# Kernel tuning notes

Hardware: AMD Instinct MI355X
Metric: run time of the kernel (lower is better)

## Reference

```python
import jax, jax.numpy as jnp
import numpy as np
from jax import lax

V_PATCH = (1, 4, 16, 64, 256, 1024)  # must end at L
RESI = 0.5    # quant_resi ratio inside Phi
BETA = 0.25
K_PHI = 4     # share_quant_resi


def _phi_indices():
    # PhiPartiallyShared tick lookup, resolved statically per scale
    K = K_PHI
    ticks = np.linspace(1/3/K, 1 - 1/3/K, K) if K == 4 else np.linspace(1/2/K, 1 - 1/2/K, K)
    SN = len(V_PATCH)
    return [int(np.argmin(np.abs(ticks - (si / (SN - 1) if SN > 1 else 0.0)))) for si in range(SN)]


def interp_linear(x, Lo):
    # torch F.interpolate(mode='linear', align_corners=False) on last axis of [B,C,Li]
    Li = x.shape[-1]
    if Li == Lo:
        return x
    pos = (jnp.arange(Lo, dtype=jnp.float32) + 0.5) * (Li / Lo) - 0.5
    pos = jnp.clip(pos, 0.0, Li - 1)
    lo = jnp.floor(pos).astype(jnp.int32)
    hi = jnp.minimum(lo + 1, Li - 1)
    w = pos - lo.astype(jnp.float32)
    return x[..., lo] * (1.0 - w) + x[..., hi] * w


def phi_apply(h, w, b):
    # Phi: h*(1-r) + Conv1d(ks=3,pad=1)(h)*r
    y = lax.conv_general_dilated(h, w, (1,), [(1, 1)], dimension_numbers=('NCH', 'OIH', 'NCH'))
    y = y + b[None, :, None]
    return h * (1.0 - RESI) + y * RESI


def reference(f_BCL, emb, phi_w, phi_b):
    f = f_BCL.astype(jnp.float32)
    B, C, L = f.shape
    f_ng = lax.stop_gradient(f)
    f_rest = f_ng
    f_hat = jnp.zeros_like(f_ng)
    SN = len(V_PATCH)
    pidx = _phi_indices()
    e_sq = jnp.sum(emb * emb, axis=1)  # [V]
    loss = jnp.float32(0.0)
    for si, pl in enumerate(V_PATCH):
        rest = interp_linear(f_rest, pl) if si != SN - 1 else f_rest
        z = rest.transpose(0, 2, 1).reshape(-1, C)              # [B*pl, C]
        d = jnp.sum(z * z, axis=1, keepdims=True) + e_sq - 2.0 * (z @ emb.T)  # [B*pl, V]
        idx = jnp.argmin(d, axis=1)
        h = emb[idx].reshape(B, pl, C).transpose(0, 2, 1)        # [B,C,pl]
        if si != SN - 1:
            h = interp_linear(h, L)
        h = phi_apply(h, phi_w[pidx[si]], phi_b[pidx[si]])
        f_hat = f_hat + h
        f_rest = f_rest - h
        loss = loss + BETA * jnp.mean((lax.stop_gradient(f_hat) - f) ** 2) \
                    + jnp.mean((f_hat - f_ng) ** 2)
    loss = loss / SN
    # straight-through estimator
    f_hat_st = lax.stop_gradient(f_hat) - f_ng + f
    return f_hat_st, loss


def setup_inputs() -> dict:
    key = jax.random.key(0)
    k1, k2, k3 = jax.random.split(key, 3)
    B, C, L, V = 32, 32, 1024, 4096
    f_BCL = jax.random.normal(k1, (B, C, L), dtype=jnp.float32)
    emb = jax.random.normal(k2, (V, C), dtype=jnp.float32)
    phi_w = jax.random.normal(k3, (K_PHI, C, C, 3), dtype=jnp.float32) * 0.05
    phi_b = jnp.zeros((K_PHI, C), dtype=jnp.float32)
    return {"f_BCL": f_BCL, "emb": emb, "phi_w": phi_w, "phi_b": phi_b}
```

## Files before the change

kernel.cpp:

```cpp
#include <hip/hip_runtime.h>
#include <stdint.h>

#define BDIM 32
#define CDIM 32
#define LDIM 1024
#define VDIM 4096
#define BCL (BDIM*CDIM*LDIM)

typedef _Float16 f16x8 __attribute__((ext_vector_type(8)));
typedef float f32x4 __attribute__((ext_vector_type(4)));

#define PIN_V(x) asm volatile("" : "+v"(x))

__global__ void init_kernel(const float* __restrict__ f, const float* __restrict__ emb,
                            float* __restrict__ f_rest, float* __restrict__ f_hat,
                            float* __restrict__ e_sq,
                            _Float16* __restrict__ eh, _Float16* __restrict__ el,
                            float* __restrict__ loss_acc, unsigned* __restrict__ done_ctr,
                            unsigned long long* __restrict__ keys, int nkeys) {
    int i = blockIdx.x * blockDim.x + threadIdx.x;
    if (i < BCL) { f_rest[i] = f[i]; f_hat[i] = 0.0f; }
    if (i < VDIM) {
        const float* e = emb + (size_t)i * CDIM;
        float s = 0.f;
#pragma unroll
        for (int k = 0; k < 32; ++k) {
            float v = e[k];
            s = fmaf(v, v, s);
            if (eh) {
                _Float16 h = (_Float16)v;
                float r = v - (float)h;
                eh[(size_t)i*32 + k] = (_Float16)(-2.0f) * h;
                el[(size_t)i*32 + k] = (_Float16)(-2.0f) * (_Float16)r;
            }
        }
        e_sq[i] = s;
    }
    if (i < nkeys) keys[i] = ~0ull;
    if (i == 0) { *loss_acc = 0.f; *done_ctr = 0u; }
}

__global__ __launch_bounds__(256) void vq_mfma(
    const _Float16* __restrict__ z_hi, const _Float16* __restrict__ z_lo,
    const _Float16* __restrict__ e_hi, const _Float16* __restrict__ e_lo,
    const float* __restrict__ e_sq, unsigned long long* __restrict__ keys,
    int NQ, int VC, int vchunks, int vsub)
{
    const int t = threadIdx.x;
    const int lane = t & 63;
    const int w = t >> 6;
    const int qg = blockIdx.x / vchunks;
    const int vc = blockIdx.x % vchunks;
    const int vb0 = vc * (vsub * VC);

    __shared__ __align__(16) _Float16 eh_ls[256*32];
    __shared__ __align__(16) _Float16 el_ls[256*32];
    __shared__ float esq_ls[256];

    const int fr = lane & 15;
    const int kq = lane >> 4;
    const int qbase = qg*256 + w*64;
    f16x8 ah[4], al[4];
#pragma unroll
    for (int tq = 0; tq < 4; ++tq) {
        int q = qbase + tq*16 + fr;
        ah[tq] = *(const f16x8*)(z_hi + (size_t)q*32 + kq*8);
        al[tq] = *(const f16x8*)(z_lo + (size_t)q*32 + kq*8);
    }

    float bd[4][4]; int bv[4][4];
#pragma unroll
    for (int tq = 0; tq < 4; ++tq)
#pragma unroll
        for (int i = 0; i < 4; ++i) { bd[tq][i] = 3.4e38f; bv[tq][i] = 0; }

    for (int sub = 0; sub < vsub; ++sub) {
        const int vb = vb0 + sub * VC;

        {
            const float4* sH = (const float4*)(e_hi + (size_t)vb*32);
            const float4* sL = (const float4*)(e_lo + (size_t)vb*32);
            float4* dH = (float4*)eh_ls; float4* dL = (float4*)el_ls;
            int n4 = VC * 4;
            for (int x = t; x < n4; x += 256) {
                int row = x >> 2, c = x & 3;
                int ds = row*4 + (c ^ ((row >> 1) & 3));
                dH[ds] = sH[x]; dL[ds] = sL[x];
            }
            for (int v = t; v < VC; v += 256) esq_ls[v] = e_sq[vb + v];
        }
        __syncthreads();

        for (int vt = 0; vt < VC; vt += 16) {
            const int row = vt + fr;
            const int koff = (kq ^ ((row >> 1) & 3)) * 8;
            const f16x8 bh = *(const f16x8*)(eh_ls + (size_t)row*32 + koff);
            const f16x8 bl = *(const f16x8*)(el_ls + (size_t)row*32 + koff);
            float es = esq_ls[row];
            int vg = vb + row;
#pragma unroll
            for (int tq = 0; tq < 4; ++tq) {
                f32x4 acc = {es, es, es, es};
                acc = __builtin_amdgcn_mfma_f32_16x16x32_f16(ah[tq], bh, acc, 0,0,0);
                acc = __builtin_amdgcn_mfma_f32_16x16x32_f16(ah[tq], bl, acc, 0,0,0);
                acc = __builtin_amdgcn_mfma_f32_16x16x32_f16(al[tq], bh, acc, 0,0,0);
#pragma unroll
                for (int i = 0; i < 4; ++i)
                    if (acc[i] < bd[tq][i]) { bd[tq][i] = acc[i]; bv[tq][i] = vg; }
            }
        }
        __syncthreads();
    }

#pragma unroll
    for (int tq = 0; tq < 4; ++tq) {
#pragma unroll
        for (int i = 0; i < 4; ++i) {
            unsigned u = __float_as_uint(bd[tq][i]);
            u = (u & 0x80000000u) ? ~u : (u | 0x80000000u);
            unsigned long long k = ((unsigned long long)u << 32) | (unsigned)bv[tq][i];
#pragma unroll
            for (int m = 1; m < 16; m <<= 1) {
                unsigned long long o = __shfl_xor(k, m, 64); if (o < k) k = o;
            }
            if (fr == 0) {
                int q = qbase + tq*16 + kq*4 + i;
                atomicMin(&keys[q], k);
            }
        }
    }
}

__global__ __launch_bounds__(256) void vq_scan(
    const float* __restrict__ f_rest, const float* __restrict__ z_buf,
    const float* __restrict__ emb, const float* __restrict__ e_sq,
    unsigned long long* __restrict__ keys,
    int lpl, int s, int NQ, int VC, int vchunks)
{
    const int pl = 1 << lpl;
    const int t  = threadIdx.x;
    const int qg = blockIdx.x / vchunks;
    const int vc = blockIdx.x % vchunks;
    const int vb = vc * VC;

    __shared__ __align__(16) float e_ls[128 * 32];
    __shared__ float esq_ls[128];

    {
        const float4* src = (const float4*)emb + (size_t)vb * 8;
        float4* dst = (float4*)e_ls;
        for (int x = t; x < VC * 8; x += 256) dst[x] = src[x];
        if (t < VC) esq_ls[t] = e_sq[vb + t];
    }

    const int q0 = qg * 512 + t;
    const int q1 = q0 + 256;
    const int qc0 = (q0 < NQ) ? q0 : NQ - 1;
    const int qc1 = (q1 < NQ) ? q1 : NQ - 1;

    float z0[32], z1[32];
    if (z_buf) {
        const float4* p0 = (const float4*)(z_buf + (size_t)qc0 * 32);
        const float4* p1 = (const float4*)(z_buf + (size_t)qc1 * 32);
#pragma unroll
        for (int c4 = 0; c4 < 8; ++c4) {
            float4 a = p0[c4], b = p1[c4];
            z0[c4*4+0] = a.x; z0[c4*4+1] = a.y; z0[c4*4+2] = a.z; z0[c4*4+3] = a.w;
            z1[c4*4+0] = b.x; z1[c4*4+1] = b.y; z1[c4*4+2] = b.z; z1[c4*4+3] = b.w;
        }
    } else {
        int b0 = qc0 >> lpl, j0 = qc0 & (pl - 1);
        int b1 = qc1 >> lpl, j1 = qc1 & (pl - 1);
        if (pl == LDIM) {
            const float* p0 = f_rest + b0 * (CDIM * LDIM) + j0;
            const float* p1 = f_rest + b1 * (CDIM * LDIM) + j1;
#pragma unroll
            for (int c = 0; c < 32; ++c) { z0[c] = p0[c * LDIM]; z1[c] = p1[c * LDIM]; }
        } else {
            int col0 = j0 * s + (s >> 1) - 1;
            int col1 = j1 * s + (s >> 1) - 1;
            const float* p0 = f_rest + b0 * (CDIM * LDIM) + col0;
            const float* p1 = f_rest + b1 * (CDIM * LDIM) + col1;
#pragma unroll
            for (int c = 0; c < 32; ++c) {
                z0[c] = 0.5f * (p0[c * LDIM] + p0[c * LDIM + 1]);
                z1[c] = 0.5f * (p1[c * LDIM] + p1[c * LDIM + 1]);
            }
        }
    }

    __syncthreads();

    float bd0 = 3.4e38f, bd1 = 3.4e38f;
    int bv0 = 0, bv1 = 0;

#pragma unroll 1
    for (int v = 0; v < VC; v += 2) {
#pragma unroll
        for (int c = 0; c < 32; ++c) { PIN_V(z0[c]); PIN_V(z1[c]); }

        const float4* er0 = (const float4*)&e_ls[(size_t)v * 32];
        const float4* er1 = er0 + 8;
        float es0 = esq_ls[v];
        float es1 = esq_ls[v + 1];

        float4 e0 = er0[0], e1 = er1[0];
        float a00 = z0[0] * e0.x,        a01 = z0[0] * e1.x;
        float a10 = z1[0] * e0.x,        a11 = z1[0] * e1.x;
        a00 = fmaf(z0[1], e0.y, a00);    a01 = fmaf(z0[1], e1.y, a01);
        a10 = fmaf(z1[1], e0.y, a10);    a11 = fmaf(z1[1], e1.y, a11);
        a00 = fmaf(z0[2], e0.z, a00);    a01 = fmaf(z0[2], e1.z, a01);
        a10 = fmaf(z1[2], e0.z, a10);    a11 = fmaf(z1[2], e1.z, a11);
        a00 = fmaf(z0[3], e0.w, a00);    a01 = fmaf(z0[3], e1.w, a01);
        a10 = fmaf(z1[3], e0.w, a10);    a11 = fmaf(z1[3], e1.w, a11);
#pragma unroll
        for (int c4 = 1; c4 < 8; ++c4) {
            e0 = er0[c4]; e1 = er1[c4];
            a00 = fmaf(z0[c4*4+0], e0.x, a00);  a01 = fmaf(z0[c4*4+0], e1.x, a01);
            a10 = fmaf(z1[c4*4+0], e0.x, a10);  a11 = fmaf(z1[c4*4+0], e1.x, a11);
            a00 = fmaf(z0[c4*4+1], e0.y, a00);  a01 = fmaf(z0[c4*4+1], e1.y, a01);
            a10 = fmaf(z1[c4*4+1], e0.y, a10);  a11 = fmaf(z1[c4*4+1], e1.y, a11);
            a00 = fmaf(z0[c4*4+2], e0.z, a00);  a01 = fmaf(z0[c4*4+2], e1.z, a01);
            a10 = fmaf(z1[c4*4+2], e0.z, a10);  a11 = fmaf(z1[c4*4+2], e1.z, a11);
            a00 = fmaf(z0[c4*4+3], e0.w, a00);  a01 = fmaf(z0[c4*4+3], e1.w, a01);
            a10 = fmaf(z1[c4*4+3], e0.w, a10);  a11 = fmaf(z1[c4*4+3], e1.w, a11);
        }
        float d00 = fmaf(a00, -2.0f, es0);
        float d01 = fmaf(a01, -2.0f, es1);
        float d10 = fmaf(a10, -2.0f, es0);
        float d11 = fmaf(a11, -2.0f, es1);
        if (d00 < bd0) { bd0 = d00; bv0 = vb + v; }
        if (d01 < bd0) { bd0 = d01; bv0 = vb + v + 1; }
        if (d10 < bd1) { bd1 = d10; bv1 = vb + v; }
        if (d11 < bd1) { bd1 = d11; bv1 = vb + v + 1; }
    }

    if (q0 < NQ) {
        unsigned ud = __float_as_uint(bd0);
        ud = (ud & 0x80000000u) ? ~ud : (ud | 0x80000000u);
        atomicMin(&keys[q0], ((unsigned long long)ud << 32) | (unsigned)bv0);
    }
    if (q1 < NQ) {
        unsigned ud = __float_as_uint(bd1);
        ud = (ud & 0x80000000u) ? ~ud : (ud | 0x80000000u);
        atomicMin(&keys[q1], ((unsigned long long)ud << 32) | (unsigned)bv1);
    }
}

__global__ __launch_bounds__(256) void fuse_kernel(
    const float* __restrict__ f, const float* __restrict__ emb,
    const unsigned long long* __restrict__ keys,
    unsigned long long* __restrict__ keys_next, int nq_next,
    _Float16* __restrict__ zh_next, _Float16* __restrict__ zl_next, int s_next,
    const float* __restrict__ w, const float* __restrict__ bias,
    float* __restrict__ f_rest, float* __restrict__ f_hat,
    float* __restrict__ loss_acc, unsigned* __restrict__ done_ctr,
    float* __restrict__ out_loss, int pl)
{
    const int t  = threadIdx.x;
    const int b  = blockIdx.y;
    const int l0 = blockIdx.x * 64;

    if (keys_next) {
        int x = (b * gridDim.x + blockIdx.x) * 256 + t;
        if (x < nq_next) keys_next[x] = ~0ull;
    }

    __shared__ float w_s[3072];
    __shared__ float b_s[32];
    __shared__ float hs[32 * 68];
    __shared__ float red[4];

    for (int x = t; x < 3072; x += 256) w_s[x] = w[x];
    if (t < 32) b_s[t] = bias[t];

    if (t < 66) {
        int l = l0 - 1 + t;
        if (l < 0 || l >= LDIM) {
#pragma unroll
            for (int i = 0; i < 32; ++i) hs[i * 68 + t] = 0.f;
        } else {
            int lo, hi; float wg;
            if (pl == LDIM) { lo = l; hi = l; wg = 0.f; }
            else {
                float pos = (l + 0.5f) * ((float)pl / 1024.0f) - 0.5f;
                pos = fminf(fmaxf(pos, 0.f), (float)(pl - 1));
                lo = (int)floorf(pos);
                hi = min(lo + 1, pl - 1);
                wg = pos - (float)lo;
            }
            int v0 = (int)(keys[b * pl + lo] & 0xFFFFFFFFull);
            int v1 = (int)(keys[b * pl + hi] & 0xFFFFFFFFull);
            const float4* e0 = (const float4*)(emb + (size_t)v0 * 32);
            const float4* e1 = (const float4*)(emb + (size_t)v1 * 32);
            float om = 1.0f - wg;
#pragma unroll
            for (int i4 = 0; i4 < 8; ++i4) {
                float4 a = e0[i4]; float4 c = e1[i4];
                hs[(i4*4+0) * 68 + t] = a.x * om + c.x * wg;
                hs[(i4*4+1) * 68 + t] = a.y * om + c.y * wg;
                hs[(i4*4+2) * 68 + t] = a.z * om + c.z * wg;
                hs[(i4*4+3) * 68 + t] = a.w * om + c.w * wg;
            }
        }
    }
    __syncthreads();

    const int o  = t >> 3;
    const int lg = t & 7;
    const float* wrow = &w_s[o * 96];
    float acc[8];
#pragma unroll
    for (int u = 0; u < 8; ++u) acc[u] = 0.f;
    const int hbase = lg * 8;

    for (int i = 0; i < 32; ++i) {
        float w0 = wrow[i * 3 + 0], w1 = wrow[i * 3 + 1], w2 = wrow[i * 3 + 2];
        const float* hrow = &hs[i * 68 + hbase];
        float hw[10];
#pragma unroll
        for (int x = 0; x < 10; ++x) hw[x] = hrow[x];
#pragma unroll
        for (int u = 0; u < 8; ++u) {
            acc[u] = fmaf(w0, hw[u], acc[u]);
            acc[u] = fmaf(w1, hw[u + 1], acc[u]);
            acc[u] = fmaf(w2, hw[u + 2], acc[u]);
        }
    }

    float lsum = 0.f;
    float frv[8];
    const int gbase = (b * 32 + o) * LDIM + l0 + lg * 8;
#pragma unroll
    for (int u = 0; u < 8; ++u) {
        float hval = hs[o * 68 + lg * 8 + 1 + u];
        float y = acc[u] + b_s[o];
        float ph = 0.5f * hval + 0.5f * y;
        int gi = gbase + u;
        float fh = f_hat[gi] + ph;
        f_hat[gi] = fh;
        float fr = f_rest[gi] - ph;
        f_rest[gi] = fr;
        frv[u] = fr;
        float df = fh - f[gi];
        lsum = fmaf(df, df, lsum);
    }

    if (zh_next) {
        __syncthreads();
#pragma unroll
        for (int u = 0; u < 8; ++u) hs[o * 68 + lg * 8 + u] = frv[u];
        __syncthreads();
        int npos = 64 / s_next;
        int qn_base = b * (LDIM / s_next) + l0 / s_next;
        for (int v = t; v < npos * 32; v += 256) {
            int jl = v >> 5, c = v & 31;
            float zv;
            if (s_next == 1) zv = hs[c * 68 + jl];
            else {
                int cl = jl * s_next + (s_next >> 1) - 1;
                zv = 0.5f * (hs[c * 68 + cl] + hs[c * 68 + cl + 1]);
            }
            _Float16 h = (_Float16)zv;
            float r = zv - (float)h;
            size_t zi = (size_t)(qn_base + jl) * 32 + c;
            zh_next[zi] = h;
            zl_next[zi] = (_Float16)r;
        }
    }

#pragma unroll
    for (int off = 32; off > 0; off >>= 1) lsum += __shfl_down(lsum, off, 64);
    if ((t & 63) == 0) red[t >> 6] = lsum;
    __syncthreads();
    if (t == 0) {
        atomicAdd(loss_acc, red[0] + red[1] + red[2] + red[3]);
        if (out_loss) {
            __threadfence();
            unsigned old = atomicAdd(done_ctr, 1u);
            if (old == (unsigned)(gridDim.x * gridDim.y - 1)) {
                float lv = atomicAdd(loss_acc, 0.0f);
                *out_loss = lv * (1.25f / (6.0f * (float)BCL));
            }
        }
    }
}

extern "C" void kernel_launch(void* const* d_in, const int* in_sizes, int n_in,
                              void* d_out, int out_size, void* d_ws, size_t ws_size,
                              hipStream_t stream)
{
    const float* f    = (const float*)d_in[0];
    const float* emb  = (const float*)d_in[1];
    const float* phiw = (const float*)d_in[2];
    const float* phib = (const float*)d_in[3];

    float* f_hat    = (float*)d_out;
    float* out_loss = f_hat + BCL;

    const int pls[6]   = {1, 4, 16, 64, 256, 1024};
    const int lpls[6]  = {0, 2, 4, 6, 8, 10};
    const int vch[6]   = {64, 64, 64, 64, 32, 32};
    const int vchm[6]  = {0, 0, 64, 16, 8, 4};
    const int vsbm[6]  = {0, 0, 1, 1, 2, 4};
    const int pidx[6]  = {0, 0, 1, 2, 3, 3};
    const int snx[6]   = {256, 64, 16, 4, 1, 0};

    char* ws = (char*)d_ws;
    float* f_rest = (float*)ws;

    size_t base = (size_t)BCL * 4;
    size_t off = base;
    unsigned long long* keysA = (unsigned long long*)(ws + off);
    unsigned long long* keysB = keysA + 32768;
    off += (size_t)65536 * 8;
    _Float16* z_hi = (_Float16*)(ws + off); off += (size_t)32768 * 32 * 2;
    _Float16* z_lo = (_Float16*)(ws + off); off += (size_t)32768 * 32 * 2;
    _Float16* e_hi = (_Float16*)(ws + off); off += (size_t)VDIM * 32 * 2;
    _Float16* e_lo = (_Float16*)(ws + off); off += (size_t)VDIM * 32 * 2;
    size_t need_mf = off + (size_t)VDIM * 4 + 64;
    bool mf = ws_size >= need_mf;

    if (!mf) {
        off = base;
        size_t need_pp = base + (size_t)65536 * 8 + (size_t)VDIM * 4 + 64;
        bool pp = ws_size >= need_pp;
        keysB = pp ? keysA + 32768 : keysA;
        off += pp ? (size_t)65536 * 8 : (size_t)32768 * 8;
        float* e_sq        = (float*)(ws + off);
        float* loss_acc    = e_sq + VDIM;
        unsigned* done_ctr = (unsigned*)(loss_acc + 1);

        init_kernel<<<dim3((BCL + 255) / 256), 256, 0, stream>>>(
            f, emb, f_rest, f_hat, e_sq, nullptr, nullptr, loss_acc, done_ctr, keysA, 32768);

        for (int si = 0; si < 6; ++si) {
            int pl = pls[si], s = LDIM / pl, NQ = BDIM * pl;
            int qgroups = (NQ + 511) >> 9;
            int VC = VDIM / vch[si];
            unsigned long long* k  = (si & 1) ? keysB : keysA;
            unsigned long long* kn = (si < 5 && pp) ? ((si & 1) ? keysA : keysB) : nullptr;
            int nq_next = (si < 5) ? BDIM * pls[si + 1] : 0;
            if (!pp && si > 0) hipMemsetAsync(k, 0xFF, (size_t)NQ * 8, stream);
            vq_scan<<<dim3(qgroups * vch[si]), 256, 0, stream>>>(
                f_rest, nullptr, emb, e_sq, k, lpls[si], s, NQ, VC, vch[si]);
            fuse_kernel<<<dim3(16, 32), 256, 0, stream>>>(
                f, emb, k, kn, nq_next, nullptr, nullptr, snx[si],
                phiw + (size_t)pidx[si] * 3072, phib + (size_t)pidx[si] * 32,
                f_rest, f_hat, loss_acc, done_ctr,
                (si == 5) ? out_loss : nullptr, pl);
        }
        return;
    }

    float* e_sq        = (float*)(ws + off);
    float* loss_acc    = e_sq + VDIM;
    unsigned* done_ctr = (unsigned*)(loss_acc + 1);

    init_kernel<<<dim3((BCL + 255) / 256), 256, 0, stream>>>(
        f, emb, f_rest, f_hat, e_sq, e_hi, e_lo, loss_acc, done_ctr, keysA, 32768);

    for (int si = 0; si < 6; ++si) {
        int pl = pls[si], s = LDIM / pl, NQ = BDIM * pl;
        unsigned long long* k  = (si & 1) ? keysB : keysA;
        unsigned long long* kn = (si < 5) ? ((si & 1) ? keysA : keysB) : nullptr;
        int nq_next = (si < 5) ? BDIM * pls[si + 1] : 0;
        if (si >= 2) {
            int vcm = vchm[si], vsb = vsbm[si];
            int VC = VDIM / (vcm * vsb);
            vq_mfma<<<dim3((NQ / 256) * vcm), 256, 0, stream>>>(
                z_hi, z_lo, e_hi, e_lo, e_sq, k, NQ, VC, vcm, vsb);
        } else {
            int qgroups = (NQ + 511) >> 9;
            vq_scan<<<dim3(qgroups * vch[si]), 256, 0, stream>>>(
                f_rest, nullptr, emb, e_sq, k, lpls[si], s, NQ, VDIM / vch[si], vch[si]);
        }
        bool zw = (si >= 1 && si <= 4);
        fuse_kernel<<<dim3(16, 32), 256, 0, stream>>>(
            f, emb, k, kn, nq_next,
            zw ? z_hi : nullptr, zw ? z_lo : nullptr, snx[si],
            phiw + (size_t)pidx[si] * 3072, phib + (size_t)pidx[si] * 32,
            f_rest, f_hat, loss_acc, done_ctr,
            (si == 5) ? out_loss : nullptr, pl);
    }
}
```

Before: 321.1 us.

## Drop init kernel; fuse embedding prep into new per-query small-scale VQ kernel

Removes the full-tensor init pass that copied f into f_rest and zeroed f_hat. The first fuse stage now reads f directly instead. A new vq_small kernel handles the first two scales with one block per query: it writes the key directly with no atomics, and extra blocks compute e_sq and the fp16 split embeddings in parallel. This cuts a memory-bound pass of about 8 MB of traffic plus a launch. The cost is that vq_small recomputes e_sq per embedding row inside its scan, and work for the tiny scales is spread over only a few blocks.

```diff
diff --git a/kernel.cpp b/kernel.cpp
--- a/kernel.cpp
+++ b/kernel.cpp
@@ -12,11 +12,16 @@
 
 #define PIN_V(x) asm volatile("" : "+v"(x))
 
+__device__ __forceinline__ unsigned long long pack_key(float bd, int bv) {
+    unsigned u = __float_as_uint(bd);
+    u = (u & 0x80000000u) ? ~u : (u | 0x80000000u);
+    return ((unsigned long long)u << 32) | (unsigned)bv;
+}
+
 __global__ void init_kernel(const float* __restrict__ f, const float* __restrict__ emb,
                             float* __restrict__ f_rest, float* __restrict__ f_hat,
-                            float* __restrict__ e_sq,
-                            _Float16* __restrict__ eh, _Float16* __restrict__ el,
-                            float* __restrict__ loss_acc, unsigned* __restrict__ done_ctr,
+                            float* __restrict__ e_sq, float* __restrict__ loss_acc,
+                            unsigned* __restrict__ done_ctr,
                             unsigned long long* __restrict__ keys, int nkeys) {
     int i = blockIdx.x * blockDim.x + threadIdx.x;
     if (i < BCL) { f_rest[i] = f[i]; f_hat[i] = 0.0f; }
@@ -24,20 +29,81 @@
         const float* e = emb + (size_t)i * CDIM;
         float s = 0.f;
 #pragma unroll
-        for (int k = 0; k < 32; ++k) {
-            float v = e[k];
-            s = fmaf(v, v, s);
-            if (eh) {
+        for (int k = 0; k < 32; ++k) { float v = e[k]; s = fmaf(v, v, s); }
+        e_sq[i] = s;
+    }
+    if (i < nkeys) keys[i] = ~0ull;
+    if (i == 0) { *loss_acc = 0.f; *done_ctr = 0u; }
+}
+
+__global__ __launch_bounds__(256) void vq_small(
+    const float* __restrict__ src, const float* __restrict__ emb,
+    _Float16* __restrict__ eh, _Float16* __restrict__ el, float* __restrict__ e_sq,
+    unsigned long long* __restrict__ keys,
+    float* __restrict__ loss_acc, unsigned* __restrict__ done_ctr,
+    int lpl, int s, int NQ)
+{
+    const int bid = blockIdx.x, t = threadIdx.x;
+    if (bid >= NQ) {
+        if (bid == NQ && t == 0) { *loss_acc = 0.f; *done_ctr = 0u; }
+        int i = (bid - NQ) * 256 + t;
+        if (i < VDIM) {
+            const float* e = emb + (size_t)i * 32;
+            float ssum = 0.f;
+#pragma unroll
+            for (int k = 0; k < 32; ++k) {
+                float v = e[k];
+                ssum = fmaf(v, v, ssum);
                 _Float16 h = (_Float16)v;
                 float r = v - (float)h;
                 eh[(size_t)i*32 + k] = (_Float16)(-2.0f) * h;
                 el[(size_t)i*32 + k] = (_Float16)(-2.0f) * (_Float16)r;
             }
-        }
-        e_sq[i] = s;
-    }
-    if (i < nkeys) keys[i] = ~0ull;
-    if (i == 0) { *loss_acc = 0.f; *done_ctr = 0u; }
+            e_sq[i] = ssum;
+        }
+        return;
+    }
+
+    const int pl = 1 << lpl;
+    const int q = bid;
+    const int b = q >> lpl, j = q & (pl - 1);
+    const int col = j * s + (s >> 1) - 1;
+    const float* p = src + b * (CDIM * LDIM) + col;
+    float z[32];
+#pragma unroll
+    for (int c = 0; c < 32; ++c) z[c] = 0.5f * (p[c * LDIM] + p[c * LDIM + 1]);
+
+    float bd = 3.4e38f; int bv = 0;
+    const int vs = t * 16;
+    for (int v = vs; v < vs + 16; ++v) {
+        const float* e = emb + (size_t)v * 32;
+        float ev[32];
+#pragma unroll
+        for (int c = 0; c < 32; ++c) ev[c] = e[c];
+        float es = 0.f;
+#pragma unroll
+        for (int c = 0; c < 32; ++c) es = fmaf(ev[c], ev[c], es);
+        float a = z[0] * ev[0];
+#pragma unroll
+        for (int c = 1; c < 32; ++c) a = fmaf(z[c], ev[c], a);
+        float d = fmaf(a, -2.0f, es);
+        if (d < bd) { bd = d; bv = v; }
+    }
+
+    unsigned long long key = pack_key(bd, bv);
+#pragma unroll
+    for (int m = 1; m < 64; m <<= 1) {
+        unsigned long long o = __shfl_xor(key, m, 64); if (o < key) key = o;
+    }
+    __shared__ unsigned long long redk[4];
+    if ((t & 63) == 0) redk[t >> 6] = key;
+    __syncthreads();
+    if (t == 0) {
+        unsigned long long kk = redk[0];
+#pragma unroll
+        for (int m = 1; m < 4; ++m) if (redk[m] < kk) kk = redk[m];
+        keys[q] = kk;
+    }
 }
 
 __global__ __launch_bounds__(256) void vq_mfma(
@@ -76,7 +142,6 @@
 
     for (int sub = 0; sub < vsub; ++sub) {
         const int vb = vb0 + sub * VC;
-
         {
             const float4* sH = (const float4*)(e_hi + (size_t)vb*32);
             const float4* sL = (const float4*)(e_lo + (size_t)vb*32);
@@ -116,23 +181,18 @@
     for (int tq = 0; tq < 4; ++tq) {
 #pragma unroll
         for (int i = 0; i < 4; ++i) {
-            unsigned u = __float_as_uint(bd[tq][i]);
-            u = (u & 0x80000000u) ? ~u : (u | 0x80000000u);
-            unsigned long long k = ((unsigned long long)u << 32) | (unsigned)bv[tq][i];
+            unsigned long long k = pack_key(bd[tq][i], bv[tq][i]);
 #pragma unroll
             for (int m = 1; m < 16; m <<= 1) {
                 unsigned long long o = __shfl_xor(k, m, 64); if (o < k) k = o;
             }
-            if (fr == 0) {
-                int q = qbase + tq*16 + kq*4 + i;
-                atomicMin(&keys[q], k);
-            }
+            if (fr == 0) atomicMin(&keys[qbase + tq*16 + kq*4 + i], k);
         }
     }
 }
 
 __global__ __launch_bounds__(256) void vq_scan(
-    const float* __restrict__ f_rest, const float* __restrict__ z_buf,
+    const float* __restrict__ f_rest,
     const float* __restrict__ emb, const float* __restrict__ e_sq,
     unsigned long long* __restrict__ keys,
     int lpl, int s, int NQ, int VC, int vchunks)
@@ -159,16 +219,7 @@
     const int qc1 = (q1 < NQ) ? q1 : NQ - 1;
 
     float z0[32], z1[32];
-    if (z_buf) {
-        const float4* p0 = (const float4*)(z_buf + (size_t)qc0 * 32);
-        const float4* p1 = (const float4*)(z_buf + (size_t)qc1 * 32);
-#pragma unroll
-        for (int c4 = 0; c4 < 8; ++c4) {
-            float4 a = p0[c4], b = p1[c4];
-            z0[c4*4+0] = a.x; z0[c4*4+1] = a.y; z0[c4*4+2] = a.z; z0[c4*4+3] = a.w;
-            z1[c4*4+0] = b.x; z1[c4*4+1] = b.y; z1[c4*4+2] = b.z; z1[c4*4+3] = b.w;
-        }
-    } else {
+    {
         int b0 = qc0 >> lpl, j0 = qc0 & (pl - 1);
         int b1 = qc1 >> lpl, j1 = qc1 & (pl - 1);
         if (pl == LDIM) {
@@ -235,16 +286,8 @@
         if (d11 < bd1) { bd1 = d11; bv1 = vb + v + 1; }
     }
 
-    if (q0 < NQ) {
-        unsigned ud = __float_as_uint(bd0);
-        ud = (ud & 0x80000000u) ? ~ud : (ud | 0x80000000u);
-        atomicMin(&keys[q0], ((unsigned long long)ud << 32) | (unsigned)bv0);
-    }
-    if (q1 < NQ) {
-        unsigned ud = __float_as_uint(bd1);
-        ud = (ud & 0x80000000u) ? ~ud : (ud | 0x80000000u);
-        atomicMin(&keys[q1], ((unsigned long long)ud << 32) | (unsigned)bv1);
-    }
+    if (q0 < NQ) atomicMin(&keys[q0], pack_key(bd0, bv0));
+    if (q1 < NQ) atomicMin(&keys[q1], pack_key(bd1, bv1));
 }
 
 __global__ __launch_bounds__(256) void fuse_kernel(
@@ -255,7 +298,7 @@
     const float* __restrict__ w, const float* __restrict__ bias,
     float* __restrict__ f_rest, float* __restrict__ f_hat,
     float* __restrict__ loss_acc, unsigned* __restrict__ done_ctr,
-    float* __restrict__ out_loss, int pl)
+    float* __restrict__ out_loss, int pl, int from_f)
 {
     const int t  = threadIdx.x;
     const int b  = blockIdx.y;
@@ -337,12 +380,13 @@
         float y = acc[u] + b_s[o];
         float ph = 0.5f * hval + 0.5f * y;
         int gi = gbase + u;
-        float fh = f_hat[gi] + ph;
+        float fv = f[gi];
+        float fh = (from_f ? 0.0f : f_hat[gi]) + ph;
         f_hat[gi] = fh;
-        float fr = f_rest[gi] - ph;
+        float fr = (from_f ? fv : f_rest[gi]) - ph;
         f_rest[gi] = fr;
         frv[u] = fr;
-        float df = fh - f[gi];
+        float df = fh - fv;
         lsum = fmaf(df, df, lsum);
     }
 
@@ -400,7 +444,6 @@
 
     const int pls[6]   = {1, 4, 16, 64, 256, 1024};
     const int lpls[6]  = {0, 2, 4, 6, 8, 10};
-    const int vch[6]   = {64, 64, 64, 64, 32, 32};
     const int vchm[6]  = {0, 0, 64, 16, 8, 4};
     const int vsbm[6]  = {0, 0, 1, 1, 2, 4};
     const int pidx[6]  = {0, 0, 1, 2, 3, 3};
@@ -421,7 +464,42 @@
     size_t need_mf = off + (size_t)VDIM * 4 + 64;
     bool mf = ws_size >= need_mf;
 
-    if (!mf) {
+    if (mf) {
+        float* e_sq        = (float*)(ws + off);
+        float* loss_acc    = e_sq + VDIM;
+        unsigned* done_ctr = (unsigned*)(loss_acc + 1);
+
+        for (int si = 0; si < 6; ++si) {
+            int pl = pls[si], s = LDIM / pl, NQ = BDIM * pl;
+            unsigned long long* k  = (si & 1) ? keysB : keysA;
+            unsigned long long* kn = (si >= 1 && si < 5) ? ((si & 1) ? keysA : keysB) : nullptr;
+            int nq_next = (si < 5) ? BDIM * pls[si + 1] : 0;
+
+            if (si <= 1) {
+                int grid = NQ + (si == 0 ? 16 : 0);
+                vq_small<<<dim3(grid), 256, 0, stream>>>(
+                    (si == 0) ? f : f_rest, emb, e_hi, e_lo, e_sq, k,
+                    loss_acc, done_ctr, lpls[si], s, NQ);
+            } else {
+                int vcm = vchm[si], vsb = vsbm[si];
+                int VC = VDIM / (vcm * vsb);
+                vq_mfma<<<dim3((NQ / 256) * vcm), 256, 0, stream>>>(
+                    z_hi, z_lo, e_hi, e_lo, e_sq, k, NQ, VC, vcm, vsb);
+            }
+
+            bool zw = (si >= 1 && si <= 4);
+            fuse_kernel<<<dim3(16, 32), 256, 0, stream>>>(
+                f, emb, k, kn, nq_next,
+                zw ? z_hi : nullptr, zw ? z_lo : nullptr, snx[si],
+                phiw + (size_t)pidx[si] * 3072, phib + (size_t)pidx[si] * 32,
+                f_rest, f_hat, loss_acc, done_ctr,
+                (si == 5) ? out_loss : nullptr, pl, (si == 0) ? 1 : 0);
+        }
+        return;
+    }
+
+    {
+        const int vch[6]  = {64, 64, 64, 64, 32, 32};
         off = base;
         size_t need_pp = base + (size_t)65536 * 8 + (size_t)VDIM * 4 + 64;
         bool pp = ws_size >= need_pp;
@@ -432,7 +510,7 @@
         unsigned* done_ctr = (unsigned*)(loss_acc + 1);
 
         init_kernel<<<dim3((BCL + 255) / 256), 256, 0, stream>>>(
-            f, emb, f_rest, f_hat, e_sq, nullptr, nullptr, loss_acc, done_ctr, keysA, 32768);
+            f, emb, f_rest, f_hat, e_sq, loss_acc, done_ctr, keysA, 32768);
 
         for (int si = 0; si < 6; ++si) {
             int pl = pls[si], s = LDIM / pl, NQ = BDIM * pl;
@@ -443,44 +521,12 @@
             int nq_next = (si < 5) ? BDIM * pls[si + 1] : 0;
             if (!pp && si > 0) hipMemsetAsync(k, 0xFF, (size_t)NQ * 8, stream);
             vq_scan<<<dim3(qgroups * vch[si]), 256, 0, stream>>>(
-                f_rest, nullptr, emb, e_sq, k, lpls[si], s, NQ, VC, vch[si]);
+                f_rest, emb, e_sq, k, lpls[si], s, NQ, VC, vch[si]);
             fuse_kernel<<<dim3(16, 32), 256, 0, stream>>>(
                 f, emb, k, kn, nq_next, nullptr, nullptr, snx[si],
                 phiw + (size_t)pidx[si] * 3072, phib + (size_t)pidx[si] * 32,
                 f_rest, f_hat, loss_acc, done_ctr,
-                (si == 5) ? out_loss : nullptr, pl);
-        }
-        return;
-    }
-
-    float* e_sq        = (float*)(ws + off);
-    float* loss_acc    = e_sq + VDIM;
-    unsigned* done_ctr = (unsigned*)(loss_acc + 1);
-
-    init_kernel<<<dim3((BCL + 255) / 256), 256, 0, stream>>>(
-        f, emb, f_rest, f_hat, e_sq, e_hi, e_lo, loss_acc, done_ctr, keysA, 32768);
-
-    for (int si = 0; si < 6; ++si) {
-        int pl = pls[si], s = LDIM / pl, NQ = BDIM * pl;
-        unsigned long long* k  = (si & 1) ? keysB : keysA;
-        unsigned long long* kn = (si < 5) ? ((si & 1) ? keysA : keysB) : nullptr;
-        int nq_next = (si < 5) ? BDIM * pls[si + 1] : 0;
-        if (si >= 2) {
-            int vcm = vchm[si], vsb = vsbm[si];
-            int VC = VDIM / (vcm * vsb);
-            vq_mfma<<<dim3((NQ / 256) * vcm), 256, 0, stream>>>(
-                z_hi, z_lo, e_hi, e_lo, e_sq, k, NQ, VC, vcm, vsb);
-        } else {
-            int qgroups = (NQ + 511) >> 9;
-            vq_scan<<<dim3(qgroups * vch[si]), 256, 0, stream>>>(
-                f_rest, nullptr, emb, e_sq, k, lpls[si], s, NQ, VDIM / vch[si], vch[si]);
-        }
-        bool zw = (si >= 1 && si <= 4);
-        fuse_kernel<<<dim3(16, 32), 256, 0, stream>>>(
-            f, emb, k, kn, nq_next,
-            zw ? z_hi : nullptr, zw ? z_lo : nullptr, snx[si],
-            phiw + (size_t)pidx[si] * 3072, phib + (size_t)pidx[si] * 32,
-            f_rest, f_hat, loss_acc, done_ctr,
-            (si == 5) ? out_loss : nullptr, pl);
-    }
-}
+                (si == 5) ? out_loss : nullptr, pl, 0);
+        }
+    }
+}
```

Measured after the change: 328.2 us. +2.2%, slower.
